# Performance work log

Measured on AMD Instinct MI355X. Metric: run time of the kernel, lower is better.

The kernel has to match this reference:

```python
import jax, jax.numpy as jnp
import numpy as np

N_NODES = 50000
N_EDGES = 800000
IN_C = 128
HID = 64          # hidden_channels
OUT_C = 128


def _glorot(key, shape):
    fan_in, fan_out = shape[1], shape[0]
    lim = (6.0 / (fan_in + fan_out)) ** 0.5
    return jax.random.uniform(key, shape, jnp.float32, -lim, lim)


def setup_inputs() -> dict:
    key = jax.random.key(0)
    ks = jax.random.split(key, 12)
    x = jax.random.normal(ks[0], (N_NODES, IN_C), jnp.float32)
    edge_index = jax.random.randint(ks[1], (2, N_EDGES), 0, N_NODES, jnp.int64)
    # SAGEConv params: lin_l (aggregated neighbors, with bias), lin_r (self, no bias)
    # layer1: 128 -> 128 (hidden*2), layer2: 128 -> 64, layer3: 64 -> 128
    d1, d2, d3 = 2 * HID, HID, OUT_C
    return {
        "x": x,
        "edge_index": edge_index,
        "W1l": _glorot(ks[2], (d1, IN_C)), "b1": jnp.zeros((d1,), jnp.float32), "W1r": _glorot(ks[3], (d1, IN_C)),
        "W2l": _glorot(ks[4], (d2, d1)),  "b2": jnp.zeros((d2,), jnp.float32), "W2r": _glorot(ks[5], (d2, d1)),
        "W3l": _glorot(ks[6], (d3, d2)),  "b3": jnp.zeros((d3,), jnp.float32), "W3r": _glorot(ks[7], (d3, d2)),
    }


def _sage_conv(x, src, dst, Wl, bl, Wr):
    # mean-aggregate source features at destination nodes (PyG SAGEConv, aggr='mean')
    msg = x[src]                                                  # [E, d]
    agg = jax.ops.segment_sum(msg, dst, num_segments=N_NODES)     # [N, d]
    cnt = jax.ops.segment_sum(jnp.ones((src.shape[0],), x.dtype), dst, num_segments=N_NODES)
    mean = agg / jnp.maximum(cnt, 1.0)[:, None]
    return mean @ Wl.T + bl + x @ Wr.T


def reference(x, edge_index, W1l, b1, W1r, W2l, b2, W2r, W3l, b3, W3r):
    src, dst = edge_index[0], edge_index[1]
    h1 = jax.nn.relu(_sage_conv(x, src, dst, W1l, b1, W1r))   # dropout: eval mode -> identity
    h2 = jax.nn.relu(_sage_conv(h1, src, dst, W2l, b2, W2r))
    h3 = jax.nn.relu(_sage_conv(h2, src, dst, W3l, b3, W3r))
    return jnp.concatenate([h1, h2, h3], axis=1)              # torch.hstack
```

## Files before the change

kernel.cpp:

```cpp
#include <hip/hip_runtime.h>
#include <hip/hip_bf16.h>

#define N_NODES 50000
#define N_EDGES 800000

constexpr int NP = 50176;
constexpr int E4 = N_EDGES / 4;
constexpr int EB4 = (E4 + 255) / 256;
constexpr int WCB = 256;
constexpr int CVB = (N_NODES * 128 / 4 + 255) / 256;

typedef __attribute__((ext_vector_type(8))) short bf16x8;
typedef __attribute__((ext_vector_type(4))) float f32x4;

__device__ __forceinline__ unsigned short f2bf(float f) {
    unsigned u = __float_as_uint(f);
    u += 0x7FFFu + ((u >> 16) & 1u);
    return (unsigned short)(u >> 16);
}

__global__ void zero_kernel(int* __restrict__ p, int n) {
    int i = blockIdx.x * 256 + threadIdx.x;
    if (i < n) p[i] = 0;
}

__global__ __launch_bounds__(256) void prep_kernel(
        const int* __restrict__ dst, int* __restrict__ cnt, int* __restrict__ pos,
        const float* __restrict__ W1l, const float* __restrict__ W1r,
        const float* __restrict__ W2l, const float* __restrict__ W2r,
        const float* __restrict__ W3l, const float* __restrict__ W3r,
        unsigned short* __restrict__ Wc1, unsigned short* __restrict__ Wc2,
        unsigned short* __restrict__ Wc3,
        const float* __restrict__ x, unsigned short* __restrict__ xb) {
    int b = blockIdx.x;
    int tid = threadIdx.x;
    if (b < EB4) {
        int t4 = b * 256 + tid;
        if (t4 < E4) {
            int4 d4 = reinterpret_cast<const int4*>(dst)[t4];
            int4 p4;
            p4.x = atomicAdd(&cnt[d4.x], 1);
            p4.y = atomicAdd(&cnt[d4.y], 1);
            p4.z = atomicAdd(&cnt[d4.z], 1);
            p4.w = atomicAdd(&cnt[d4.w], 1);
            reinterpret_cast<int4*>(pos)[t4] = p4;
        }
    } else if (b < EB4 + WCB) {
        int idx = (b - EB4) * 256 + tid;
        if (idx < 32768) {
            int nr = idx >> 8, k = idx & 255;
            float v = (k < 128) ? W1l[nr * 128 + k] : W1r[nr * 128 + (k - 128)];
            Wc1[idx] = f2bf(v);
        } else if (idx < 49152) {
            int j = idx - 32768;
            int nr = j >> 8, k = j & 255;
            float v = (k < 128) ? W2l[nr * 128 + k] : W2r[nr * 128 + (k - 128)];
            Wc2[j] = f2bf(v);
        } else {
            int j = idx - 49152;
            int nr = j >> 7, k = j & 127;
            float v = (k < 64) ? W3l[nr * 64 + k] : W3r[nr * 64 + (k - 64)];
            Wc3[j] = f2bf(v);
        }
    } else {
        int i = (b - EB4 - WCB) * 256 + tid;
        if (i < N_NODES * 128 / 4) {
            float4 v = reinterpret_cast<const float4*>(x)[i];
            uint2 p;
            p.x = (unsigned)f2bf(v.x) | ((unsigned)f2bf(v.y) << 16);
            p.y = (unsigned)f2bf(v.z) | ((unsigned)f2bf(v.w) << 16);
            reinterpret_cast<uint2*>(xb)[i] = p;
        }
    }
}

__global__ void assign_kernel(const int* __restrict__ cnt, int* __restrict__ row_ptr,
                              float* __restrict__ inv_deg, int* __restrict__ total, int n) {
    int i = blockIdx.x * blockDim.x + threadIdx.x;
    int lane = threadIdx.x & 63;
    int v = (i < n) ? cnt[i] : 0;
    int s = v;
    #pragma unroll
    for (int off = 1; off < 64; off <<= 1) {
        int t = __shfl_up(s, off);
        if (lane >= off) s += t;
    }
    int base = 0;
    if (lane == 63) base = atomicAdd(total, s);
    base = __shfl(base, 63);
    if (i < n) {
        row_ptr[i] = base + s - v;
        inv_deg[i] = 1.0f / (float)(v > 1 ? v : 1);
    }
}

__global__ void fill_kernel(const int* __restrict__ src, const int* __restrict__ dst,
                            const int* __restrict__ row_ptr,
                            const int* __restrict__ pos, int* __restrict__ edge_src) {
    int t4 = blockIdx.x * 256 + threadIdx.x;
    if (t4 < E4) {
        int4 s4 = reinterpret_cast<const int4*>(src)[t4];
        int4 d4 = reinterpret_cast<const int4*>(dst)[t4];
        int4 p4 = reinterpret_cast<const int4*>(pos)[t4];
        edge_src[row_ptr[d4.x] + p4.x] = s4.x;
        edge_src[row_ptr[d4.y] + p4.y] = s4.y;
        edge_src[row_ptr[d4.z] + p4.z] = s4.z;
        edge_src[row_ptr[d4.w] + p4.w] = s4.w;
    }
}

template<int D>
__global__ __launch_bounds__(256) void agg_kernel(
        const unsigned short* __restrict__ hb,
        const int* __restrict__ row_ptr, const int* __restrict__ cnt,
        const int* __restrict__ edge_src,
        const float* __restrict__ inv_deg, unsigned short* __restrict__ meanb, int n) {
    constexpr int LPR = D / 8;
    constexpr int EPW = 64 / LPR;
    int wid = (blockIdx.x * 256 + threadIdx.x) >> 6;
    int lane = threadIdx.x & 63;
    if (wid >= n) return;
    int beg = row_ptr[wid];
    int end = beg + cnt[wid];
    float inv = inv_deg[wid];
    int sub = lane / LPR;
    int li = lane % LPR;

    float acc[8];
    #pragma unroll
    for (int j = 0; j < 8; ++j) acc[j] = 0.f;

    for (int e0 = beg; e0 < end; e0 += 4 * EPW) {
        int ea = e0 + sub;
        int eb = ea + EPW;
        int ec = ea + 2 * EPW;
        int ed = ea + 3 * EPW;
        uint4 v0 = {0u,0u,0u,0u}, v1 = {0u,0u,0u,0u}, v2 = {0u,0u,0u,0u}, v3 = {0u,0u,0u,0u};
        if (ea < end) v0 = *reinterpret_cast<const uint4*>(hb + (size_t)edge_src[ea] * D + li * 8);
        if (eb < end) v1 = *reinterpret_cast<const uint4*>(hb + (size_t)edge_src[eb] * D + li * 8);
        if (ec < end) v2 = *reinterpret_cast<const uint4*>(hb + (size_t)edge_src[ec] * D + li * 8);
        if (ed < end) v3 = *reinterpret_cast<const uint4*>(hb + (size_t)edge_src[ed] * D + li * 8);
        unsigned w;
        #define ACCW(u, j0) w = (u); acc[j0] += __uint_as_float(w << 16); acc[j0+1] += __uint_as_float(w & 0xFFFF0000u)
        ACCW(v0.x, 0); ACCW(v0.y, 2); ACCW(v0.z, 4); ACCW(v0.w, 6);
        ACCW(v1.x, 0); ACCW(v1.y, 2); ACCW(v1.z, 4); ACCW(v1.w, 6);
        ACCW(v2.x, 0); ACCW(v2.y, 2); ACCW(v2.z, 4); ACCW(v2.w, 6);
        ACCW(v3.x, 0); ACCW(v3.y, 2); ACCW(v3.z, 4); ACCW(v3.w, 6);
        #undef ACCW
    }
    #pragma unroll
    for (int off = LPR; off < 64; off <<= 1) {
        #pragma unroll
        for (int j = 0; j < 8; ++j) acc[j] += __shfl_xor(acc[j], off);
    }
    if (lane < LPR) {
        uint4 w;
        w.x = (unsigned)f2bf(acc[0] * inv) | ((unsigned)f2bf(acc[1] * inv) << 16);
        w.y = (unsigned)f2bf(acc[2] * inv) | ((unsigned)f2bf(acc[3] * inv) << 16);
        w.z = (unsigned)f2bf(acc[4] * inv) | ((unsigned)f2bf(acc[5] * inv) << 16);
        w.w = (unsigned)f2bf(acc[6] * inv) | ((unsigned)f2bf(acc[7] * inv) << 16);
        *reinterpret_cast<uint4*>(meanb + (size_t)wid * D + li * 8) = w;
    }
}

template<int K, int DOUT, bool WB>
__global__ __launch_bounds__(256, 3) void mfma_gemm_kernel(
        const unsigned short* __restrict__ Ab,
        const unsigned short* __restrict__ Fb,
        const unsigned short* __restrict__ Wc,
        const float* __restrict__ bias,
        float* __restrict__ out, int outs,
        unsigned short* __restrict__ outb, int n) {
    constexpr int DIN = K / 2;
    constexpr int KK = K / 32;
    constexpr int NWC = DOUT / 32;
    constexpr int NWM = 4 / NWC;
    constexpr int GW = 4;
    constexpr int BM = 16 * GW * NWM;
    int wave = threadIdx.x >> 6;
    int lane = threadIdx.x & 63;
    int wc = wave % NWC;
    int wm = wave / NWC;
    int arow = lane & 15;
    int kseg = lane >> 4;

    bf16x8 b0[KK], b1[KK];
    {
        const unsigned short* wp0 = Wc + (size_t)(wc * 32 + arow) * K + kseg * 8;
        const unsigned short* wp1 = wp0 + (size_t)16 * K;
        #pragma unroll
        for (int kk = 0; kk < KK; ++kk) {
            b0[kk] = *reinterpret_cast<const bf16x8*>(wp0 + kk * 32);
            b1[kk] = *reinterpret_cast<const bf16x8*>(wp1 + kk * 32);
        }
    }
    float bv0 = bias[wc * 32 + arow];
    float bv1 = bias[wc * 32 + 16 + arow];

    int g0 = blockIdx.x * (BM / 16) + wm * GW;

    bf16x8 a0[KK], a1[KK];

    #define LOADA(g, dst)                                                          \
    {                                                                              \
        int node = (g0 + (g)) * 16 + arow;                                         \
        int ncl = node < n ? node : 0;                                             \
        _Pragma("unroll")                                                          \
        for (int kk = 0; kk < KK; ++kk) {                                          \
            int k = kk * 32 + kseg * 8;                                            \
            const unsigned short* p = (k < DIN) ? (Ab + (size_t)ncl * DIN + k)     \
                                                : (Fb + (size_t)ncl * DIN + (k - DIN)); \
            dst[kk] = *reinterpret_cast<const bf16x8*>(p);                         \
        }                                                                          \
    }

    #define COMPUTE(g, ab)                                                         \
    {                                                                              \
        f32x4 acc0 = {0.f, 0.f, 0.f, 0.f}, acc1 = {0.f, 0.f, 0.f, 0.f};           \
        _Pragma("unroll")                                                          \
        for (int kk = 0; kk < KK; ++kk) {                                          \
            acc0 = __builtin_amdgcn_mfma_f32_16x16x32_bf16(ab[kk], b0[kk], acc0, 0, 0, 0); \
            acc1 = __builtin_amdgcn_mfma_f32_16x16x32_bf16(ab[kk], b1[kk], acc1, 0, 0, 0); \
        }                                                                          \
        int gbase = (g0 + (g)) * 16 + kseg * 4;                                    \
        _Pragma("unroll")                                                          \
        for (int r = 0; r < 4; ++r) {                                              \
            int gn = gbase + r;                                                    \
            if (gn < n) {                                                          \
                int col0 = wc * 32 + arow;                                         \
                float v0 = fmaxf(acc0[r] + bv0, 0.f);                              \
                float v1 = fmaxf(acc1[r] + bv1, 0.f);                              \
                out[(size_t)gn * outs + col0] = v0;                                \
                out[(size_t)gn * outs + col0 + 16] = v1;                           \
                if constexpr (WB) {                                                \
                    outb[(size_t)gn * DOUT + col0] = f2bf(v0);                     \
                    outb[(size_t)gn * DOUT + col0 + 16] = f2bf(v1);                \
                }                                                                  \
            }                                                                      \
        }                                                                          \
    }

    LOADA(0, a0);
    #pragma unroll
    for (int gp = 0; gp < GW; gp += 2) {
        LOADA(gp + 1, a1);
        COMPUTE(gp, a0);
        if (gp + 2 < GW) LOADA(gp + 2, a0);
        COMPUTE(gp + 1, a1);
    }
    #undef LOADA
    #undef COMPUTE
}

extern "C" void kernel_launch(void* const* d_in, const int* in_sizes, int n_in,
                              void* d_out, int out_size, void* d_ws, size_t ws_size,
                              hipStream_t stream) {
    const float* x   = (const float*)d_in[0];
    const int*   ei  = (const int*)d_in[1];
    const float* W1l = (const float*)d_in[2];
    const float* b1  = (const float*)d_in[3];
    const float* W1r = (const float*)d_in[4];
    const float* W2l = (const float*)d_in[5];
    const float* b2  = (const float*)d_in[6];
    const float* W2r = (const float*)d_in[7];
    const float* W3l = (const float*)d_in[8];
    const float* b3  = (const float*)d_in[9];
    const float* W3r = (const float*)d_in[10];
    float* out = (float*)d_out;

    const int* src = ei;
    const int* dst = ei + N_EDGES;

    int* wsi = (int*)d_ws;
    int*   cnt      = wsi;
    int*   total    = wsi + NP;
    int*   row_ptr  = wsi + NP + 64;
    float* inv_deg  = (float*)(wsi + 2 * NP + 64);
    int*   edge_src = wsi + 3 * NP + 64;
    int*   pos      = edge_src + N_EDGES;
    unsigned short* Wc1 = (unsigned short*)(pos + N_EDGES);
    unsigned short* Wc2 = Wc1 + 128 * 256;
    unsigned short* Wc3 = Wc2 + 64 * 256;
    unsigned short* meanb = Wc3 + 128 * 128;
    unsigned short* xb  = meanb + (size_t)N_NODES * 128;
    unsigned short* h1b = xb + (size_t)N_NODES * 128;
    unsigned short* h2b = h1b + (size_t)N_NODES * 128;

    zero_kernel<<<(NP + 64 + 255) / 256, 256, 0, stream>>>(cnt, NP + 64);

    prep_kernel<<<EB4 + WCB + CVB, 256, 0, stream>>>(dst, cnt, pos,
        W1l, W1r, W2l, W2r, W3l, W3r, Wc1, Wc2, Wc3, x, xb);

    assign_kernel<<<NP / 256, 256, 0, stream>>>(cnt, row_ptr, inv_deg, total, N_NODES);
    fill_kernel<<<EB4, 256, 0, stream>>>(src, dst, row_ptr, pos, edge_src);

    const int AGG_BLOCKS = (N_NODES + 3) / 4;
    const int GB64  = (N_NODES + 63) / 64;
    const int GB128 = (N_NODES + 127) / 128;

    agg_kernel<128><<<AGG_BLOCKS, 256, 0, stream>>>(xb, row_ptr, cnt, edge_src, inv_deg, meanb, N_NODES);
    mfma_gemm_kernel<256, 128, true><<<GB64, 256, 0, stream>>>(meanb, xb, Wc1, b1, out, 320, h1b, N_NODES);

    agg_kernel<128><<<AGG_BLOCKS, 256, 0, stream>>>(h1b, row_ptr, cnt, edge_src, inv_deg, meanb, N_NODES);
    mfma_gemm_kernel<256, 64, true><<<GB128, 256, 0, stream>>>(meanb, h1b, Wc2, b2, out + 128, 320, h2b, N_NODES);

    agg_kernel<64><<<AGG_BLOCKS, 256, 0, stream>>>(h2b, row_ptr, cnt, edge_src, inv_deg, meanb, N_NODES);
    mfma_gemm_kernel<128, 128, false><<<GB64, 256, 0, stream>>>(meanb, h2b, Wc3, b3, out + 192, 320, nullptr, N_NODES);
}
```

Measured before the change: 221.3 us.

## Transform layer-1 features before aggregation and fuse bias/ReLU into aggregation epilogue

Layer 1 now uses linearity of the mean: x is multiplied by W1l and W1r inside the prep kernel using MFMA. The aggregation kernel gathers the transformed rows and adds the self term plus bias, then applies ReLU and writes both the fp32 output and the bf16 h1. This removes the separate x-to-bf16 conversion pass and the first GEMM launch. The cost is that prep now does the dense GEMM inline and stores two 128-wide bf16 intermediates, with extra rounding before aggregation and per-element scalar stores.

```diff
diff --git a/kernel.cpp b/kernel.cpp
--- a/kernel.cpp
+++ b/kernel.cpp
@@ -6,9 +6,10 @@
 
 constexpr int NP = 50176;
 constexpr int E4 = N_EDGES / 4;
-constexpr int EB4 = (E4 + 255) / 256;
-constexpr int WCB = 256;
-constexpr int CVB = (N_NODES * 128 / 4 + 255) / 256;
+constexpr int E8 = N_EDGES / 8;
+constexpr int ATB = (E8 + 255) / 256;
+constexpr int PGB = (N_NODES + 63) / 64;
+constexpr int WCB2 = (64 * 256 + 128 * 128) / 256;
 
 typedef __attribute__((ext_vector_type(8))) short bf16x8;
 typedef __attribute__((ext_vector_type(4))) float f32x4;
@@ -19,6 +20,15 @@
     return (unsigned short)(u >> 16);
 }
 
+__device__ __forceinline__ bf16x8 pack8(float4 f0, float4 f1) {
+    bf16x8 r;
+    r[0] = (short)f2bf(f0.x); r[1] = (short)f2bf(f0.y);
+    r[2] = (short)f2bf(f0.z); r[3] = (short)f2bf(f0.w);
+    r[4] = (short)f2bf(f1.x); r[5] = (short)f2bf(f1.y);
+    r[6] = (short)f2bf(f1.z); r[7] = (short)f2bf(f1.w);
+    return r;
+}
+
 __global__ void zero_kernel(int* __restrict__ p, int n) {
     int i = blockIdx.x * 256 + threadIdx.x;
     if (i < n) p[i] = 0;
@@ -26,50 +36,101 @@
 
 __global__ __launch_bounds__(256) void prep_kernel(
         const int* __restrict__ dst, int* __restrict__ cnt, int* __restrict__ pos,
-        const float* __restrict__ W1l, const float* __restrict__ W1r,
+        const float* __restrict__ x,
+        const float* __restrict__ W1l, const float* __restrict__ b1,
+        const float* __restrict__ W1r,
         const float* __restrict__ W2l, const float* __restrict__ W2r,
         const float* __restrict__ W3l, const float* __restrict__ W3r,
-        unsigned short* __restrict__ Wc1, unsigned short* __restrict__ Wc2,
-        unsigned short* __restrict__ Wc3,
-        const float* __restrict__ x, unsigned short* __restrict__ xb) {
+        unsigned short* __restrict__ xlb, unsigned short* __restrict__ s1b,
+        unsigned short* __restrict__ Wc2, unsigned short* __restrict__ Wc3) {
     int b = blockIdx.x;
     int tid = threadIdx.x;
-    if (b < EB4) {
-        int t4 = b * 256 + tid;
-        if (t4 < E4) {
-            int4 d4 = reinterpret_cast<const int4*>(dst)[t4];
-            int4 p4;
-            p4.x = atomicAdd(&cnt[d4.x], 1);
-            p4.y = atomicAdd(&cnt[d4.y], 1);
-            p4.z = atomicAdd(&cnt[d4.z], 1);
-            p4.w = atomicAdd(&cnt[d4.w], 1);
-            reinterpret_cast<int4*>(pos)[t4] = p4;
-        }
-    } else if (b < EB4 + WCB) {
-        int idx = (b - EB4) * 256 + tid;
-        if (idx < 32768) {
+    if (b < ATB) {
+        int t8 = b * 256 + tid;
+        if (t8 < E8) {
+            int4 d0 = reinterpret_cast<const int4*>(dst)[t8 * 2];
+            int4 d1 = reinterpret_cast<const int4*>(dst)[t8 * 2 + 1];
+            int4 p0, p1;
+            p0.x = atomicAdd(&cnt[d0.x], 1);
+            p0.y = atomicAdd(&cnt[d0.y], 1);
+            p0.z = atomicAdd(&cnt[d0.z], 1);
+            p0.w = atomicAdd(&cnt[d0.w], 1);
+            p1.x = atomicAdd(&cnt[d1.x], 1);
+            p1.y = atomicAdd(&cnt[d1.y], 1);
+            p1.z = atomicAdd(&cnt[d1.z], 1);
+            p1.w = atomicAdd(&cnt[d1.w], 1);
+            reinterpret_cast<int4*>(pos)[t8 * 2] = p0;
+            reinterpret_cast<int4*>(pos)[t8 * 2 + 1] = p1;
+        }
+    } else if (b < ATB + PGB) {
+        int pb = b - ATB;
+        int wave = tid >> 6;
+        int lane = tid & 63;
+        int arow = lane & 15;
+        int kseg = lane >> 4;
+        bf16x8 bw[4][4];
+        float bias_v[4];
+        #pragma unroll
+        for (int t = 0; t < 4; ++t) {
+            int col = wave * 64 + t * 16 + arow;
+            const float* wrow = (col < 128) ? (W1l + (size_t)col * 128)
+                                            : (W1r + (size_t)(col - 128) * 128);
+            bias_v[t] = (col < 128) ? 0.f : b1[col - 128];
+            #pragma unroll
+            for (int kk = 0; kk < 4; ++kk) {
+                int k = kk * 32 + kseg * 8;
+                float4 f0 = *reinterpret_cast<const float4*>(wrow + k);
+                float4 f1 = *reinterpret_cast<const float4*>(wrow + k + 4);
+                bw[t][kk] = pack8(f0, f1);
+            }
+        }
+        for (int g = 0; g < 4; ++g) {
+            int node = pb * 64 + g * 16 + arow;
+            int ncl = node < N_NODES ? node : 0;
+            bf16x8 a[4];
+            #pragma unroll
+            for (int kk = 0; kk < 4; ++kk) {
+                const float* xr = x + (size_t)ncl * 128 + kk * 32 + kseg * 8;
+                float4 f0 = *reinterpret_cast<const float4*>(xr);
+                float4 f1 = *reinterpret_cast<const float4*>(xr + 4);
+                a[kk] = pack8(f0, f1);
+            }
+            f32x4 acc0 = {0.f,0.f,0.f,0.f}, acc1 = {0.f,0.f,0.f,0.f};
+            f32x4 acc2 = {0.f,0.f,0.f,0.f}, acc3 = {0.f,0.f,0.f,0.f};
+            #pragma unroll
+            for (int kk = 0; kk < 4; ++kk) {
+                acc0 = __builtin_amdgcn_mfma_f32_16x16x32_bf16(a[kk], bw[0][kk], acc0, 0, 0, 0);
+                acc1 = __builtin_amdgcn_mfma_f32_16x16x32_bf16(a[kk], bw[1][kk], acc1, 0, 0, 0);
+                acc2 = __builtin_amdgcn_mfma_f32_16x16x32_bf16(a[kk], bw[2][kk], acc2, 0, 0, 0);
+                acc3 = __builtin_amdgcn_mfma_f32_16x16x32_bf16(a[kk], bw[3][kk], acc3, 0, 0, 0);
+            }
+            int gn0 = pb * 64 + g * 16 + kseg * 4;
+            #pragma unroll
+            for (int r = 0; r < 4; ++r) {
+                int gn = gn0 + r;
+                if (gn < N_NODES) {
+                    #pragma unroll
+                    for (int t = 0; t < 4; ++t) {
+                        int col = wave * 64 + t * 16 + arow;
+                        float v = (t == 0 ? acc0[r] : t == 1 ? acc1[r] : t == 2 ? acc2[r] : acc3[r])
+                                  + bias_v[t];
+                        if (col < 128) xlb[(size_t)gn * 128 + col] = f2bf(v);
+                        else           s1b[(size_t)gn * 128 + (col - 128)] = f2bf(v);
+                    }
+                }
+            }
+        }
+    } else {
+        int idx = (b - ATB - PGB) * 256 + tid;
+        if (idx < 16384) {
             int nr = idx >> 8, k = idx & 255;
-            float v = (k < 128) ? W1l[nr * 128 + k] : W1r[nr * 128 + (k - 128)];
-            Wc1[idx] = f2bf(v);
-        } else if (idx < 49152) {
-            int j = idx - 32768;
-            int nr = j >> 8, k = j & 255;
             float v = (k < 128) ? W2l[nr * 128 + k] : W2r[nr * 128 + (k - 128)];
-            Wc2[j] = f2bf(v);
+            Wc2[idx] = f2bf(v);
         } else {
-            int j = idx - 49152;
+            int j = idx - 16384;
             int nr = j >> 7, k = j & 127;
             float v = (k < 64) ? W3l[nr * 64 + k] : W3r[nr * 64 + (k - 64)];
             Wc3[j] = f2bf(v);
-        }
-    } else {
-        int i = (b - EB4 - WCB) * 256 + tid;
-        if (i < N_NODES * 128 / 4) {
-            float4 v = reinterpret_cast<const float4*>(x)[i];
-            uint2 p;
-            p.x = (unsigned)f2bf(v.x) | ((unsigned)f2bf(v.y) << 16);
-            p.y = (unsigned)f2bf(v.z) | ((unsigned)f2bf(v.w) << 16);
-            reinterpret_cast<uint2*>(xb)[i] = p;
         }
     }
 }
@@ -109,12 +170,15 @@
     }
 }
 
-template<int D>
+template<int D, int MODE>
 __global__ __launch_bounds__(256) void agg_kernel(
         const unsigned short* __restrict__ hb,
         const int* __restrict__ row_ptr, const int* __restrict__ cnt,
         const int* __restrict__ edge_src,
-        const float* __restrict__ inv_deg, unsigned short* __restrict__ meanb, int n) {
+        const float* __restrict__ inv_deg,
+        unsigned short* __restrict__ meanb,
+        const unsigned short* __restrict__ s1b,
+        float* __restrict__ outF, unsigned short* __restrict__ h1b, int n) {
     constexpr int LPR = D / 8;
     constexpr int EPW = 64 / LPR;
     int wid = (blockIdx.x * 256 + threadIdx.x) >> 6;
@@ -154,12 +218,36 @@
         for (int j = 0; j < 8; ++j) acc[j] += __shfl_xor(acc[j], off);
     }
     if (lane < LPR) {
-        uint4 w;
-        w.x = (unsigned)f2bf(acc[0] * inv) | ((unsigned)f2bf(acc[1] * inv) << 16);
-        w.y = (unsigned)f2bf(acc[2] * inv) | ((unsigned)f2bf(acc[3] * inv) << 16);
-        w.z = (unsigned)f2bf(acc[4] * inv) | ((unsigned)f2bf(acc[5] * inv) << 16);
-        w.w = (unsigned)f2bf(acc[6] * inv) | ((unsigned)f2bf(acc[7] * inv) << 16);
-        *reinterpret_cast<uint4*>(meanb + (size_t)wid * D + li * 8) = w;
+        if constexpr (MODE == 0) {
+            uint4 w;
+            w.x = (unsigned)f2bf(acc[0] * inv) | ((unsigned)f2bf(acc[1] * inv) << 16);
+            w.y = (unsigned)f2bf(acc[2] * inv) | ((unsigned)f2bf(acc[3] * inv) << 16);
+            w.z = (unsigned)f2bf(acc[4] * inv) | ((unsigned)f2bf(acc[5] * inv) << 16);
+            w.w = (unsigned)f2bf(acc[6] * inv) | ((unsigned)f2bf(acc[7] * inv) << 16);
+            *reinterpret_cast<uint4*>(meanb + (size_t)wid * D + li * 8) = w;
+        } else {
+            uint4 s4 = *reinterpret_cast<const uint4*>(s1b + (size_t)wid * 128 + li * 8);
+            float v[8];
+            v[0] = fmaxf(acc[0] * inv + __uint_as_float(s4.x << 16), 0.f);
+            v[1] = fmaxf(acc[1] * inv + __uint_as_float(s4.x & 0xFFFF0000u), 0.f);
+            v[2] = fmaxf(acc[2] * inv + __uint_as_float(s4.y << 16), 0.f);
+            v[3] = fmaxf(acc[3] * inv + __uint_as_float(s4.y & 0xFFFF0000u), 0.f);
+            v[4] = fmaxf(acc[4] * inv + __uint_as_float(s4.z << 16), 0.f);
+            v[5] = fmaxf(acc[5] * inv + __uint_as_float(s4.z & 0xFFFF0000u), 0.f);
+            v[6] = fmaxf(acc[6] * inv + __uint_as_float(s4.w << 16), 0.f);
+            v[7] = fmaxf(acc[7] * inv + __uint_as_float(s4.w & 0xFFFF0000u), 0.f);
+            float4 r0 = {v[0], v[1], v[2], v[3]};
+            float4 r1 = {v[4], v[5], v[6], v[7]};
+            float* op = outF + (size_t)wid * 320 + li * 8;
+            *reinterpret_cast<float4*>(op) = r0;
+            *reinterpret_cast<float4*>(op + 4) = r1;
+            uint4 w;
+            w.x = (unsigned)f2bf(v[0]) | ((unsigned)f2bf(v[1]) << 16);
+            w.y = (unsigned)f2bf(v[2]) | ((unsigned)f2bf(v[3]) << 16);
+            w.z = (unsigned)f2bf(v[4]) | ((unsigned)f2bf(v[5]) << 16);
+            w.w = (unsigned)f2bf(v[6]) | ((unsigned)f2bf(v[7]) << 16);
+            *reinterpret_cast<uint4*>(h1b + (size_t)wid * 128 + li * 8) = w;
+        }
     }
 }
 
@@ -278,32 +366,36 @@
     float* inv_deg  = (float*)(wsi + 2 * NP + 64);
     int*   edge_src = wsi + 3 * NP + 64;
     int*   pos      = edge_src + N_EDGES;
-    unsigned short* Wc1 = (unsigned short*)(pos + N_EDGES);
-    unsigned short* Wc2 = Wc1 + 128 * 256;
+    unsigned short* Wc2 = (unsigned short*)(pos + N_EDGES);
     unsigned short* Wc3 = Wc2 + 64 * 256;
     unsigned short* meanb = Wc3 + 128 * 128;
-    unsigned short* xb  = meanb + (size_t)N_NODES * 128;
-    unsigned short* h1b = xb + (size_t)N_NODES * 128;
+    unsigned short* xlb = meanb + (size_t)N_NODES * 128;
+    unsigned short* s1b = xlb + (size_t)N_NODES * 128;
+    unsigned short* h1b = s1b + (size_t)N_NODES * 128;
     unsigned short* h2b = h1b + (size_t)N_NODES * 128;
 
     zero_kernel<<<(NP + 64 + 255) / 256, 256, 0, stream>>>(cnt, NP + 64);
 
-    prep_kernel<<<EB4 + WCB + CVB, 256, 0, stream>>>(dst, cnt, pos,
-        W1l, W1r, W2l, W2r, W3l, W3r, Wc1, Wc2, Wc3, x, xb);
+    prep_kernel<<<ATB + PGB + WCB2, 256, 0, stream>>>(dst, cnt, pos, x,
+        W1l, b1, W1r, W2l, W2r, W3l, W3r, xlb, s1b, Wc2, Wc3);
 
     assign_kernel<<<NP / 256, 256, 0, stream>>>(cnt, row_ptr, inv_deg, total, N_NODES);
-    fill_kernel<<<EB4, 256, 0, stream>>>(src, dst, row_ptr, pos, edge_src);
+    fill_kernel<<<(E4 + 255) / 256, 256, 0, stream>>>(src, dst, row_ptr, pos, edge_src);
 
     const int AGG_BLOCKS = (N_NODES + 3) / 4;
+    const int GB128 = (N_NODES + 127) / 128;
     const int GB64  = (N_NODES + 63) / 64;
-    const int GB128 = (N_NODES + 127) / 128;
-
-    agg_kernel<128><<<AGG_BLOCKS, 256, 0, stream>>>(xb, row_ptr, cnt, edge_src, inv_deg, meanb, N_NODES);
-    mfma_gemm_kernel<256, 128, true><<<GB64, 256, 0, stream>>>(meanb, xb, Wc1, b1, out, 320, h1b, N_NODES);
-
-    agg_kernel<128><<<AGG_BLOCKS, 256, 0, stream>>>(h1b, row_ptr, cnt, edge_src, inv_deg, meanb, N_NODES);
-    mfma_gemm_kernel<256, 64, true><<<GB128, 256, 0, stream>>>(meanb, h1b, Wc2, b2, out + 128, 320, h2b, N_NODES);
-
-    agg_kernel<64><<<AGG_BLOCKS, 256, 0, stream>>>(h2b, row_ptr, cnt, edge_src, inv_deg, meanb, N_NODES);
-    mfma_gemm_kernel<128, 128, false><<<GB64, 256, 0, stream>>>(meanb, h2b, Wc3, b3, out + 192, 320, nullptr, N_NODES);
-}
+
+    agg_kernel<128, 1><<<AGG_BLOCKS, 256, 0, stream>>>(xlb, row_ptr, cnt, edge_src,
+        inv_deg, nullptr, s1b, out, h1b, N_NODES);
+
+    agg_kernel<128, 0><<<AGG_BLOCKS, 256, 0, stream>>>(h1b, row_ptr, cnt, edge_src,
+        inv_deg, meanb, nullptr, nullptr, nullptr, N_NODES);
+    mfma_gemm_kernel<256, 64, true><<<GB128, 256, 0, stream>>>(meanb, h1b, Wc2, b2,
+        out + 128, 320, h2b, N_NODES);
+
+    agg_kernel<64, 0><<<AGG_BLOCKS, 256, 0, stream>>>(h2b, row_ptr, cnt, edge_src,
+        inv_deg, meanb, nullptr, nullptr, nullptr, N_NODES);
+    mfma_gemm_kernel<128, 128, false><<<GB64, 256, 0, stream>>>(meanb, h2b, Wc3, b3,
+        out + 192, 320, nullptr, N_NODES);
+}
```

Result: no change. 222.0 us (+0.3%).
